# Kernel tuning notes

Hardware: AMD Instinct MI355X
Metric: run time of the kernel (lower is better)

The kernel has to match this reference:

```python
import jax, jax.numpy as jnp
import numpy as np

T = 5
EPS = 1e-05


def setup_inputs() -> dict:
    key = jax.random.key(0)
    X = jax.random.normal(key, (64, 512, 32, 32), dtype=jnp.float32)
    return {"X": X}


def reference(X):
    # IterNorm (training branch): whiten channels via Newton-Schulz inverse sqrt.
    N, C, H, W = X.shape
    x = jnp.transpose(X, (1, 0, 2, 3)).reshape(C, -1)  # [d, m], d=C, m=N*H*W
    d, m = x.shape
    mean = jnp.mean(x, axis=-1, keepdims=True)
    xc = x - mean
    I = jnp.eye(d, dtype=X.dtype)
    # Sigma = eps*I + (1/m) xc xc^T  (addmm(eps, I, 1/m, xc, xc^T))
    Sigma = EPS * I + (xc @ xc.T) / m
    rTr = 1.0 / jnp.trace(Sigma)          # (Sigma * I).sum().reciprocal()
    Sigma_N = Sigma * rTr
    P = I
    for _ in range(T):
        # P_{k+1} = 1.5*P_k - 0.5 * P_k^3 @ Sigma_N
        P = 1.5 * P - 0.5 * (P @ P @ P) @ Sigma_N
    wm = P * jnp.sqrt(rTr)                # whitening matrix ~ Sigma^{-1/2}
    xn = wm @ xc                          # [d, m]
    Xn = jnp.transpose(xn.reshape(C, N, H, W), (1, 0, 2, 3))
    return Xn
```

## Files before the change

kernel.cpp:

```cpp
#include <hip/hip_runtime.h>
#include <math.h>

#define Nn   64
#define Cc   512
#define HWs  1024
#define CHW  (Cc * HWs)
#define Mm   (Nn * HWs)
#define EPSC 1e-5f
#define NBC  128

typedef unsigned int   u32;
typedef unsigned short u16;
typedef __attribute__((ext_vector_type(8))) short  short8;
typedef __attribute__((ext_vector_type(4))) float  floatx4;

__device__ __forceinline__ u16 f2bf(float f) {
    u32 u = __float_as_uint(f);
    u += 0x7fff + ((u >> 16) & 1);
    return (u16)(u >> 16);
}
__device__ __forceinline__ float bf2f(u16 h) {
    return __uint_as_float(((u32)h) << 16);
}

__device__ __forceinline__ void gld_lds16(const u16* g, u16* l) {
    __builtin_amdgcn_global_load_lds(
        (const __attribute__((address_space(1))) u32*)g,
        (__attribute__((address_space(3))) u32*)l, 16, 0, 0);
}

__global__ __launch_bounds__(256) void convert_transpose(const float* __restrict__ X,
                                                         u16* __restrict__ Xbf,
                                                         u16* __restrict__ Xt,
                                                         float* __restrict__ meanP) {
    const int hT = blockIdx.x;
    const int h0 = hT << 6;
    const int c0 = blockIdx.y << 6;
    const int n  = blockIdx.z;
    const int t  = threadIdx.x;
    __shared__ u16   T[64][65];
    __shared__ float red[64][17];

    const float* Xn  = X   + (size_t)n * CHW;
    u16*         Xbn = Xbf + (size_t)n * CHW;
    u16*         Xtn = Xt  + (size_t)n * CHW;

    const int cl = t >> 4;
    const int h4 = (t & 15) << 2;
#pragma unroll
    for (int i = 0; i < 4; ++i) {
        const int c = cl + (i << 4);
        float4 v = *(const float4*)&Xn[(size_t)(c0 + c) * HWs + h0 + h4];
        red[c][t & 15] = v.x + v.y + v.z + v.w;
        u16 b0 = f2bf(v.x), b1 = f2bf(v.y), b2 = f2bf(v.z), b3 = f2bf(v.w);
        *(ushort4*)&Xbn[(size_t)(c0 + c) * HWs + h0 + h4] = make_ushort4(b0, b1, b2, b3);
        T[c][h4]     = b0;
        T[c][h4 + 1] = b1;
        T[c][h4 + 2] = b2;
        T[c][h4 + 3] = b3;
    }
    __syncthreads();
    const int hl = t >> 4;
    const int c4 = (t & 15) << 2;
#pragma unroll
    for (int i = 0; i < 4; ++i) {
        const int h = hl + (i << 4);
        ushort4 pk = make_ushort4(T[c4][h], T[c4 + 1][h], T[c4 + 2][h], T[c4 + 3][h]);
        *(ushort4*)&Xtn[(size_t)(h0 + h) * Cc + c0 + c4] = pk;
    }
    if (t < 64) {
        float s = 0.f;
#pragma unroll
        for (int j = 0; j < 16; ++j) s += red[t][j];
        atomicAdd(&meanP[hT * 512 + c0 + t], s);
    }
}

__global__ __launch_bounds__(256) void gram_mfma(const u16* __restrict__ Xbf,
                                                 float* __restrict__ G) {
    static const int TI[10] = {0,0,0,0,1,1,1,2,2,3};
    static const int TJ[10] = {0,1,2,3,1,2,3,2,3,3};
    const int id = blockIdx.x;
    const int q  = id >> 3;
    const int x  = q % 10;
    const int y  = (id & 7) + ((q / 10) << 3);
    const int i0 = TI[x] << 7;
    const int j0 = TJ[x] << 7;
    const int n  = y;
    const int t  = threadIdx.x;
    const int w  = t >> 6, l = t & 63;

    __shared__ u16 As[2][4096];
    __shared__ u16 Bs[2][4096];

    floatx4 acc[4][4];
#pragma unroll
    for (int mi = 0; mi < 4; ++mi)
#pragma unroll
        for (int ni = 0; ni < 4; ++ni) acc[mi][ni] = (floatx4){0.f, 0.f, 0.f, 0.f};

    const int lr = l >> 2;
    const int lc = (l & 3) << 3;
    const int wm = w >> 1, wn = w & 1;
    const int fm = l & 15, fq = l >> 4;

    const u16* Xn = Xbf + (size_t)n * CHW;

    auto issue = [&](int k, int bb) {
#pragma unroll
        for (int p = 0; p < 2; ++p) {
            const int g   = w * 2 + p;
            const int row = g * 16 + lr;
            gld_lds16(Xn + (size_t)(i0 + row) * HWs + (k << 5) + lc, &As[bb][g * 512]);
            gld_lds16(Xn + (size_t)(j0 + row) * HWs + (k << 5) + lc, &Bs[bb][g * 512]);
        }
    };

    issue(0, 0);
    __syncthreads();
    for (int k = 0; k < 32; ++k) {
        if (k < 31) issue(k + 1, (k + 1) & 1);
        const int bb = k & 1;
        short8 a[4], b[4];
#pragma unroll
        for (int mi = 0; mi < 4; ++mi)
            a[mi] = *(const short8*)&As[bb][(wm * 64 + mi * 16 + fm) * 32 + fq * 8];
#pragma unroll
        for (int ni = 0; ni < 4; ++ni)
            b[ni] = *(const short8*)&Bs[bb][(wn * 64 + ni * 16 + fm) * 32 + fq * 8];
#pragma unroll
        for (int mi = 0; mi < 4; ++mi)
#pragma unroll
            for (int ni = 0; ni < 4; ++ni)
                acc[mi][ni] = __builtin_amdgcn_mfma_f32_16x16x32_bf16(
                    a[mi], b[ni], acc[mi][ni], 0, 0, 0);
        __syncthreads();
    }
#pragma unroll
    for (int mi = 0; mi < 4; ++mi)
#pragma unroll
        for (int ni = 0; ni < 4; ++ni)
#pragma unroll
            for (int r = 0; r < 4; ++r) {
                const int gi = i0 + wm * 64 + mi * 16 + fq * 4 + r;
                const int gj = j0 + wn * 64 + ni * 16 + fm;
                atomicAdd(&G[(size_t)gi * Cc + gj], acc[mi][ni][r]);
            }
}

__device__ __forceinline__ void gridbar(int* bar, int gen) {
    __syncthreads();
    if (threadIdx.x == 0) {
        __threadfence();
        __hip_atomic_fetch_add(bar, 1, __ATOMIC_RELAXED, __HIP_MEMORY_SCOPE_AGENT);
        while (__hip_atomic_load(bar, __ATOMIC_RELAXED, __HIP_MEMORY_SCOPE_AGENT) < gen * NBC)
            __builtin_amdgcn_s_sleep(1);
        __threadfence();
    }
    __syncthreads();
}

template <int MR>
__device__ __forceinline__ void mm_bk64(const u16* Ah, const u16* Al,
                                        const u16* Bh, const u16* Bl,
                                        int i0, int j0,
                                        float alpha, const float* D, float beta,
                                        float* Cf, u16* Ch, u16* Cl, u16* S) {
    const int t = threadIdx.x, w = t >> 6, l = t & 63;
    const int wm = w >> 1, wn = w & 1, fm = l & 15, fq = l >> 4;
    const int lr = l >> 2, lc = (l & 3) << 3;
    constexpr int MI     = MR / 32;
    constexpr int OFF_AL = MR * 64;
    constexpr int OFF_BH = 2 * MR * 64;
    constexpr int OFF_BL = 2 * MR * 64 + 4096;
    constexpr int BUFSZ  = 2 * MR * 64 + 8192;

    const u16* src  = (w == 0) ? Ah : (w == 1) ? Al : (w == 2) ? Bh : Bl;
    const int rbase = (w < 2) ? i0 : j0;
    const int R     = (w < 2) ? MR : 64;
    const int OFF   = (w == 0) ? 0 : (w == 1) ? OFF_AL : (w == 2) ? OFF_BH : OFF_BL;

    floatx4 acc[MI][2];
#pragma unroll
    for (int mi = 0; mi < MI; ++mi)
#pragma unroll
        for (int ni = 0; ni < 2; ++ni) acc[mi][ni] = (floatx4){0.f, 0.f, 0.f, 0.f};

    auto issue = [&](int c, int bb) {
        u16* dst = S + bb * BUFSZ + OFF;
        const u16* sp = src + (size_t)rbase * 512 + (c << 6);
#pragma unroll
        for (int s = 0; s < 2; ++s)
#pragma unroll 4
            for (int g = 0; g < (R >> 4); ++g)
                gld_lds16(sp + (size_t)(g * 16 + lr) * 512 + s * 32 + lc,
                          dst + s * R * 32 + g * 512);
    };
    auto compute = [&](int bb) {
        const u16* base = S + bb * BUFSZ;
#pragma unroll
        for (int s = 0; s < 2; ++s) {
            short8 ah[MI], al[MI], bh[2], bl[2];
#pragma unroll
            for (int mi = 0; mi < MI; ++mi) {
                const int r = wm * (MR / 2) + mi * 16 + fm;
                const int o = s * MR * 32 + r * 32 + fq * 8;
                ah[mi] = *(const short8*)&base[o];
                al[mi] = *(const short8*)&base[OFF_AL + o];
            }
#pragma unroll
            for (int ni = 0; ni < 2; ++ni) {
                const int r = wn * 32 + ni * 16 + fm;
                const int o = s * 2048 + r * 32 + fq * 8;
                bh[ni] = *(const short8*)&base[OFF_BH + o];
                bl[ni] = *(const short8*)&base[OFF_BL + o];
            }
#pragma unroll
            for (int mi = 0; mi < MI; ++mi)
#pragma unroll
                for (int ni = 0; ni < 2; ++ni) {
                    acc[mi][ni] = __builtin_amdgcn_mfma_f32_16x16x32_bf16(ah[mi], bh[ni], acc[mi][ni], 0, 0, 0);
                    acc[mi][ni] = __builtin_amdgcn_mfma_f32_16x16x32_bf16(ah[mi], bl[ni], acc[mi][ni], 0, 0, 0);
                    acc[mi][ni] = __builtin_amdgcn_mfma_f32_16x16x32_bf16(al[mi], bh[ni], acc[mi][ni], 0, 0, 0);
                }
        }
    };

    issue(0, 0);
    __syncthreads();
    for (int c = 0; c < 8; ++c) {
        if (c < 7) issue(c + 1, (c + 1) & 1);
        compute(c & 1);
        __syncthreads();
    }

#pragma unroll
    for (int mi = 0; mi < MI; ++mi)
#pragma unroll
        for (int ni = 0; ni < 2; ++ni)
#pragma unroll
            for (int r4 = 0; r4 < 4; ++r4) {
                const int gi = i0 + wm * (MR / 2) + mi * 16 + fq * 4 + r4;
                const int gj = j0 + wn * 32 + ni * 16 + fm;
                const size_t idx = (size_t)gi * 512 + gj;
                float v = alpha * acc[mi][ni][r4];
                if (D) v += beta * D[idx];
                if (Cf) Cf[idx] = v;
                const u16 h = f2bf(v);
                Ch[idx] = h;
                Cl[idx] = f2bf(v - bf2f(h));
            }
}

__global__ __launch_bounds__(256) void ns_chain(
    const float* G, const float* meanP, float* scal, int* bar, float* wmmv,
    u16* Sh, u16* Sl, u16* PhA, u16* PlA, u16* PhB, u16* PlB,
    u16* T2h, u16* T2l, u16* Wh, u16* Wl, float* PfA, float* PfB) {
    __shared__ u16   S[32768];
    __shared__ float meanL[512];
    __shared__ float redL[4];
    const int t = threadIdx.x, b = blockIdx.x;
    const int w = t >> 6, l = t & 63;

    float tp = 0.f;
#pragma unroll
    for (int cb = 0; cb < 2; ++cb) {
        const int c = t + (cb << 8);
        float s = 0.f;
#pragma unroll
        for (int q = 0; q < 16; ++q) s += meanP[(q << 9) + c];
        const float mc = s * (1.0f / Mm);
        meanL[c] = mc;
        tp += G[(size_t)c * 513] * (1.0f / Mm) - mc * mc;
    }
#pragma unroll
    for (int o = 32; o > 0; o >>= 1) tp += __shfl_xor(tp, o);
    if (l == 0) redL[w] = tp;
    __syncthreads();
    const float tr  = redL[0] + redL[1] + redL[2] + redL[3] + (float)Cc * EPSC;
    const float rtr = 1.0f / tr;
    const float sr  = sqrtf(rtr);
    if (b == 0 && t == 0) { scal[0] = rtr; scal[1] = sr; }

#pragma unroll
    for (int k2 = 0; k2 < 8; ++k2) {
        const int e = (b << 11) + (k2 << 8) + t;
        const int i = e >> 9, j = e & 511;
        const float g = (i <= j) ? G[((size_t)i << 9) + j] : G[((size_t)j << 9) + i];
        float sig = g * (1.0f / Mm) - meanL[i] * meanL[j];
        if (i == j) sig += EPSC;
        const float sN = sig * rtr;
        const u16 sh = f2bf(sN);
        Sh[e] = sh;
        Sl[e] = f2bf(sN - bf2f(sh));
        const float p1 = ((i == j) ? 1.5f : 0.f) - 0.5f * sN;
        PfA[e] = p1;
        const u16 ph = f2bf(p1);
        PhA[e] = ph;
        PlA[e] = f2bf(p1 - bf2f(ph));
    }
    int gen = 0;
    gridbar(bar, ++gen);

    u16 *ph = PhA, *pl = PlA, *qh = PhB, *ql = PlB;
    float *pf = PfA, *qf = PfB;
    const int i0a = ((b & 63) >> 3) << 6, j0a = (b & 7) << 6;
    const int i0b = (b >> 3) << 5,        j0b = (b & 7) << 6;
    for (int it = 0; it < 4; ++it) {
        if (b < 64)
            mm_bk64<64>(ph, pl, ph, pl, i0a, j0a, 1.f, nullptr, 0.f,
                        nullptr, T2h, T2l, S);
        else
            mm_bk64<64>(ph, pl, Sh, Sl, i0a, j0a, 1.f, nullptr, 0.f,
                        nullptr, Wh, Wl, S);
        gridbar(bar, ++gen);
        mm_bk64<32>(T2h, T2l, Wh, Wl, i0b, j0b, -0.5f, pf, 1.5f,
                    qf, qh, ql, S);
        gridbar(bar, ++gen);
        { u16* x = ph; ph = qh; qh = x; }
        { u16* x = pl; pl = ql; ql = x; }
        { float* x = pf; pf = qf; qf = x; }
    }

    {
        const int c = (b << 2) + (t >> 6);
        float s = 0.f;
#pragma unroll
        for (int jj = 0; jj < 8; ++jj) {
            const int j = l + (jj << 6);
            s += pf[((size_t)c << 9) + j] * meanL[j];
        }
#pragma unroll
        for (int o = 32; o > 0; o >>= 1) s += __shfl_xor(s, o);
        if (l == 0) wmmv[c] = s * sr;
    }
}

__global__ __launch_bounds__(256) void whiten_mfma(const u16* __restrict__ Xt,
                                                   const u16* __restrict__ Pbf,
                                                   const float* __restrict__ wmm,
                                                   const float* __restrict__ scal,
                                                   float* __restrict__ out) {
    const int id  = blockIdx.x;
    const int m   = (id >> 3) & 3;
    const int grp = (id & 7) + ((id >> 5) << 3);
    const int c0  = m << 7;
    const int h0  = (grp & 7) << 7;
    const int n   = grp >> 3;
    const int t   = threadIdx.x;
    const int w   = t >> 6, l = t & 63;

    __shared__ char smem[128 * 68 * 4];
    u16* AsB = (u16*)smem;
    u16* BsB = AsB + 8192;
    float* Ep = (float*)smem;

    floatx4 acc[4][4];
#pragma unroll
    for (int mi = 0; mi < 4; ++mi)
#pragma unroll
        for (int ni = 0; ni < 4; ++ni) acc[mi][ni] = (floatx4){0.f, 0.f, 0.f, 0.f};

    const int lr = l >> 2;
    const int lc = (l & 3) << 3;
    const int wm = w >> 1, wn = w & 1;
    const int fm = l & 15, fq = l >> 4;

    const u16* Xn = Xt + (size_t)n * CHW;

    auto issue = [&](int k, int bb) {
#pragma unroll
        for (int p = 0; p < 2; ++p) {
            const int g   = w * 2 + p;
            const int row = g * 16 + lr;
            gld_lds16(Xn  + (size_t)(h0 + row) * Cc + (k << 5) + lc, &AsB[bb * 4096 + g * 512]);
            gld_lds16(Pbf + (size_t)(c0 + row) * Cc + (k << 5) + lc, &BsB[bb * 4096 + g * 512]);
        }
    };

    issue(0, 0);
    __syncthreads();
    for (int k = 0; k < 16; ++k) {
        if (k < 15) issue(k + 1, (k + 1) & 1);
        const int bb = k & 1;
        short8 a[4], b[4];
#pragma unroll
        for (int mi = 0; mi < 4; ++mi)
            a[mi] = *(const short8*)&AsB[bb * 4096 + (wm * 64 + mi * 16 + fm) * 32 + fq * 8];
#pragma unroll
        for (int ni = 0; ni < 4; ++ni)
            b[ni] = *(const short8*)&BsB[bb * 4096 + (wn * 64 + ni * 16 + fm) * 32 + fq * 8];
#pragma unroll
        for (int mi = 0; mi < 4; ++mi)
#pragma unroll
            for (int ni = 0; ni < 4; ++ni)
                acc[mi][ni] = __builtin_amdgcn_mfma_f32_16x16x32_bf16(
                    a[mi], b[ni], acc[mi][ni], 0, 0, 0);
        __syncthreads();
    }

    const float sr = scal[1];
    float wv[4];
#pragma unroll
    for (int ni = 0; ni < 4; ++ni) wv[ni] = wmm[c0 + wn * 64 + ni * 16 + fm];
    float* outn = out + (size_t)n * CHW;

#pragma unroll
    for (int mp = 0; mp < 2; ++mp) {
        __syncthreads();
#pragma unroll
        for (int p = 0; p < 2; ++p) {
            const int mi = mp * 2 + p;
#pragma unroll
            for (int ni = 0; ni < 4; ++ni) {
                const int row  = wn * 64 + ni * 16 + fm;
                const int slot = wm * 32 + p * 16 + fq * 4;
                floatx4 v = acc[mi][ni] * sr - wv[ni];
                *(floatx4*)&Ep[row * 68 + slot] = v;
            }
        }
        __syncthreads();
#pragma unroll
        for (int jj = 0; jj < 8; ++jj) {
            const int idx = jj * 256 + t;
            const int row = idx >> 4;
            const int s4  = (idx & 15) << 2;
            const int wmr = s4 >> 5;
            const int within = s4 & 31;
            float4 v = *(const float4*)&Ep[row * 68 + s4];
            *(float4*)&outn[(size_t)(c0 + row) * HWs + h0 + wmr * 64 + mp * 32 + within] = v;
        }
    }
}

__global__ __launch_bounds__(256) void mean_kernel(const float* __restrict__ X,
                                                   float* __restrict__ mean) {
    const int c = blockIdx.x;
    const int t = threadIdx.x;
    float s = 0.f;
    for (int n = 0; n < Nn; ++n) {
        const float4* p = (const float4*)(X + (size_t)n * CHW + (size_t)c * HWs);
        float4 v = p[t];
        s += v.x + v.y + v.z + v.w;
    }
    __shared__ float red[256];
    red[t] = s;
    __syncthreads();
    for (int o = 128; o > 0; o >>= 1) {
        if (t < o) red[t] += red[t + o];
        __syncthreads();
    }
    if (t == 0) mean[c] = red[0] * (1.0f / Mm);
}

__global__ __launch_bounds__(256) void trace_fb(const float* __restrict__ G,
                                                const float* __restrict__ mean,
                                                float* __restrict__ scal) {
    const int t = threadIdx.x;
    float s = 0.f;
    for (int i = t; i < Cc; i += 256)
        s += G[(size_t)i * Cc + i] * (1.0f / Mm) - mean[i] * mean[i];
    __shared__ float red[256];
    red[t] = s;
    __syncthreads();
    for (int o = 128; o > 0; o >>= 1) {
        if (t < o) red[t] += red[t + o];
        __syncthreads();
    }
    if (t == 0) {
        const float tr  = red[0] + (float)Cc * EPSC;
        const float rtr = 1.0f / tr;
        scal[0] = rtr;
        scal[1] = sqrtf(rtr);
    }
}

__global__ __launch_bounds__(256) void gram_kernel(const float* __restrict__ X,
                                                   float* __restrict__ G) {
    const int ti = blockIdx.x >> 3, tj = blockIdx.x & 7;
    const int i0 = ti << 6, j0 = tj << 6;
    const int n0 = blockIdx.y << 3;
    const int t  = threadIdx.x;
    const int tx = t & 15, ty = t >> 4;
    __shared__ float As[64][33];
    __shared__ float Bs[64][33];
    float acc[4][4] = {};
    const int lc = t & 31;
    const int lr0 = t >> 5;
    for (int n = n0; n < n0 + 8; ++n) {
        const float* Xn = X + (size_t)n * CHW;
        for (int hw0 = 0; hw0 < HWs; hw0 += 32) {
#pragma unroll
            for (int r = 0; r < 8; ++r) {
                const int row = lr0 + (r << 3);
                As[row][lc] = Xn[(size_t)(i0 + row) * HWs + hw0 + lc];
                Bs[row][lc] = Xn[(size_t)(j0 + row) * HWs + hw0 + lc];
            }
            __syncthreads();
#pragma unroll
            for (int k = 0; k < 32; ++k) {
                float a[4], b[4];
#pragma unroll
                for (int r = 0; r < 4; ++r) a[r] = As[(ty << 2) + r][k];
#pragma unroll
                for (int cn = 0; cn < 4; ++cn) b[cn] = Bs[(tx << 2) + cn][k];
#pragma unroll
                for (int r = 0; r < 4; ++r)
#pragma unroll
                    for (int cn = 0; cn < 4; ++cn) acc[r][cn] += a[r] * b[cn];
            }
            __syncthreads();
        }
    }
#pragma unroll
    for (int r = 0; r < 4; ++r)
#pragma unroll
        for (int cn = 0; cn < 4; ++cn)
            atomicAdd(&G[(size_t)(i0 + (ty << 2) + r) * Cc + j0 + (tx << 2) + cn],
                      acc[r][cn]);
}

__global__ __launch_bounds__(256) void sigman_full_kernel(const float* __restrict__ G,
                                                          const float* __restrict__ mean,
                                                          const float* __restrict__ scal,
                                                          float* __restrict__ S,
                                                          float* __restrict__ P) {
    const int e = blockIdx.x * 256 + threadIdx.x;
    const int i = e >> 9, j = e & 511;
    const float rtr = scal[0];
    float sig = G[e] * (1.0f / Mm) - mean[i] * mean[j];
    if (i == j) sig += EPSC;
    S[e] = sig * rtr;
    P[e] = (i == j) ? 1.f : 0.f;
}

__global__ __launch_bounds__(256) void mm512_kernel(const float* __restrict__ A,
                                                    const float* __restrict__ B,
                                                    float* __restrict__ C,
                                                    float alpha,
                                                    const float* __restrict__ D,
                                                    float beta) {
    const int ti = blockIdx.x >> 3, tj = blockIdx.x & 7;
    const int i0 = ti << 6, j0 = tj << 6;
    const int t  = threadIdx.x;
    const int tx = t & 15, ty = t >> 4;
    __shared__ float As[64][33];
    __shared__ float Bs[32][65];
    float acc[4][4] = {};
    const int lcA = t & 31, lrA = t >> 5;
    const int lcB = t & 63, lrB = t >> 6;
    for (int k0 = 0; k0 < 512; k0 += 32) {
#pragma unroll
        for (int r = 0; r < 8; ++r) {
            const int row = lrA + (r << 3);
            As[row][lcA] = A[(size_t)(i0 + row) * 512 + k0 + lcA];
        }
#pragma unroll
        for (int r = 0; r < 8; ++r) {
            const int row = lrB + (r << 2);
            Bs[row][lcB] = B[(size_t)(k0 + row) * 512 + j0 + lcB];
        }
        __syncthreads();
#pragma unroll
        for (int k = 0; k < 32; ++k) {
            float a[4], b[4];
#pragma unroll
            for (int r = 0; r < 4; ++r) a[r] = As[(ty << 2) + r][k];
#pragma unroll
            for (int cn = 0; cn < 4; ++cn) b[cn] = Bs[k][(tx << 2) + cn];
#pragma unroll
            for (int r = 0; r < 4; ++r)
#pragma unroll
                for (int cn = 0; cn < 4; ++cn) acc[r][cn] += a[r] * b[cn];
        }
        __syncthreads();
    }
#pragma unroll
    for (int r = 0; r < 4; ++r) {
        const size_t idx = (size_t)(i0 + (ty << 2) + r) * 512 + j0 + (tx << 2);
        float4 v;
        v.x = alpha * acc[r][0];
        v.y = alpha * acc[r][1];
        v.z = alpha * acc[r][2];
        v.w = alpha * acc[r][3];
        if (D) {
            const float4 d = *(const float4*)(D + idx);
            v.x += beta * d.x; v.y += beta * d.y; v.z += beta * d.z; v.w += beta * d.w;
        }
        *(float4*)(C + idx) = v;
    }
}

__global__ __launch_bounds__(128) void wmm_kernel(const float* __restrict__ P,
                                                  const float* __restrict__ mean,
                                                  const float* __restrict__ scal,
                                                  float* __restrict__ wmm) {
    const int c = blockIdx.x, t = threadIdx.x;
    float s = 0.f;
    for (int j = t; j < Cc; j += 128) s += P[(size_t)c * Cc + j] * mean[j];
    __shared__ float red[128];
    red[t] = s;
    __syncthreads();
    for (int o = 64; o > 0; o >>= 1) {
        if (t < o) red[t] += red[t + o];
        __syncthreads();
    }
    if (t == 0) wmm[c] = red[0] * scal[1];
}

__global__ __launch_bounds__(256) void whiten_kernel(const float* __restrict__ X,
                                                     const float* __restrict__ P,
                                                     const float* __restrict__ wmm,
                                                     const float* __restrict__ scal,
                                                     float* __restrict__ out) {
    const int c0 = blockIdx.x << 6;
    const int h0 = blockIdx.y << 6;
    const int n  = blockIdx.z;
    const int t  = threadIdx.x;
    const int tx = t & 15, ty = t >> 4;
    __shared__ float Ps[64][33];
    __shared__ float Xs[32][65];
    float acc[4][4] = {};
    const int lcA = t & 31, lrA = t >> 5;
    const int lcB = t & 63, lrB = t >> 6;
    const float* Xn = X + (size_t)n * CHW;
    for (int k0 = 0; k0 < 512; k0 += 32) {
#pragma unroll
        for (int r = 0; r < 8; ++r) {
            const int row = lrA + (r << 3);
            Ps[row][lcA] = P[(size_t)(c0 + row) * 512 + k0 + lcA];
        }
#pragma unroll
        for (int r = 0; r < 8; ++r) {
            const int row = lrB + (r << 2);
            Xs[row][lcB] = Xn[(size_t)(k0 + row) * HWs + h0 + lcB];
        }
        __syncthreads();
#pragma unroll
        for (int k = 0; k < 32; ++k) {
            float a[4], b[4];
#pragma unroll
            for (int r = 0; r < 4; ++r) a[r] = Ps[(ty << 2) + r][k];
#pragma unroll
            for (int cn = 0; cn < 4; ++cn) b[cn] = Xs[k][(tx << 2) + cn];
#pragma unroll
            for (int r = 0; r < 4; ++r)
#pragma unroll
                for (int cn = 0; cn < 4; ++cn) acc[r][cn] += a[r] * b[cn];
        }
        __syncthreads();
    }
    const float sr = scal[1];
#pragma unroll
    for (int r = 0; r < 4; ++r) {
        const int c = c0 + (ty << 2) + r;
        const float wv = wmm[c];
        float4 v;
        v.x = sr * acc[r][0] - wv;
        v.y = sr * acc[r][1] - wv;
        v.z = sr * acc[r][2] - wv;
        v.w = sr * acc[r][3] - wv;
        *(float4*)(out + (size_t)n * CHW + (size_t)c * HWs + h0 + (tx << 2)) = v;
    }
}

extern "C" void kernel_launch(void* const* d_in, const int* in_sizes, int n_in,
                              void* d_out, int out_size, void* d_ws, size_t ws_size,
                              hipStream_t stream) {
    const float* X = (const float*)d_in[0];
    float* out     = (float*)d_out;

    const size_t NU16 = 33554432;
    const size_t NM   = 262144;
    const size_t NEED = NU16 * 2 * 2
                      + NM * 10 * 2
                      + (NM + 8192 + 32 + 512 + 512 + 2 * NM) * 4;

    if (ws_size >= NEED) {
        u16* Xbf = (u16*)d_ws;
        u16* Xt  = Xbf + NU16;
        u16* Sh  = Xt  + NU16;
        u16* Sl  = Sh + NM;
        u16* PhA = Sl + NM;
        u16* PlA = PhA + NM;
        u16* PhB = PlA + NM;
        u16* PlB = PhB + NM;
        u16* T2h = PlB + NM;
        u16* T2l = T2h + NM;
        u16* Wh  = T2l + NM;
        u16* Wl  = Wh + NM;
        float* G     = (float*)(Wl + NM);
        float* meanP = G + NM;
        float* scal  = meanP + 8192;
        int*   bar   = (int*)(scal + 16);
        float* mean  = (float*)(bar + 16);
        float* wmm   = mean + 512;
        float* PfA   = wmm + 512;
        float* PfB   = PfA + NM;

        hipMemsetAsync(G, 0, (NM + 8192 + 32) * sizeof(float), stream);
        convert_transpose<<<dim3(16, 8, 64), 256, 0, stream>>>(X, Xbf, Xt, meanP);
        gram_mfma<<<640, 256, 0, stream>>>(Xbf, G);
        ns_chain<<<NBC, 256, 0, stream>>>(G, meanP, scal, bar, wmm,
                                          Sh, Sl, PhA, PlA, PhB, PlB,
                                          T2h, T2l, Wh, Wl, PfA, PfB);
        whiten_mfma<<<2048, 256, 0, stream>>>(Xt, PhA, wmm, scal, out);
    } else {
        float* ws   = (float*)d_ws;
        float* mean = ws;
        float* wmm  = ws + 512;
        float* scal = ws + 1024;
        float* G    = ws + 2048;
        float* S    = G + 262144;
        float* Pa   = S + 262144;
        float* Pb   = Pa + 262144;
        float* P2   = Pb + 262144;
        float* P3   = P2 + 262144;

        mean_kernel<<<512, 256, 0, stream>>>(X, mean);
        hipMemsetAsync(G, 0, sizeof(float) * 262144, stream);
        gram_kernel<<<dim3(64, 8), 256, 0, stream>>>(X, G);
        trace_fb<<<1, 256, 0, stream>>>(G, mean, scal);
        sigman_full_kernel<<<1024, 256, 0, stream>>>(G, mean, scal, S, Pa);

        float* P  = Pa;
        float* Pn = Pb;
        for (int it = 0; it < 5; ++it) {
            mm512_kernel<<<64, 256, 0, stream>>>(P, P, P2, 1.f, nullptr, 0.f);
            mm512_kernel<<<64, 256, 0, stream>>>(P2, P, P3, 1.f, nullptr, 0.f);
            mm512_kernel<<<64, 256, 0, stream>>>(P3, S, Pn, -0.5f, P, 1.5f);
            float* tmp = P; P = Pn; Pn = tmp;
        }

        wmm_kernel<<<512, 128, 0, stream>>>(P, mean, scal, wmm);
        whiten_kernel<<<dim3(8, 16, 64), 256, 0, stream>>>(X, P, wmm, scal, out);
    }
}
```

Measured before the change: 524.0 us.

## Replace grid-barrier fences with cache-bypassing loads/stores and packed transposed stores

```diff
diff --git a/kernel.cpp b/kernel.cpp
--- a/kernel.cpp
+++ b/kernel.cpp
@@ -11,6 +11,7 @@
 
 typedef unsigned int   u32;
 typedef unsigned short u16;
+typedef unsigned long long u64;
 typedef __attribute__((ext_vector_type(8))) short  short8;
 typedef __attribute__((ext_vector_type(4))) float  floatx4;
 
@@ -27,6 +28,21 @@
     __builtin_amdgcn_global_load_lds(
         (const __attribute__((address_space(1))) u32*)g,
         (__attribute__((address_space(3))) u32*)l, 16, 0, 0);
+}
+
+#define AUX_SC 0x11
+
+__device__ __forceinline__ void gld_lds16_sc(const u16* g, u16* l) {
+    __builtin_amdgcn_global_load_lds(
+        (const __attribute__((address_space(1))) u32*)g,
+        (__attribute__((address_space(3))) u32*)l, 16, 0, AUX_SC);
+}
+__device__ __forceinline__ void st8_sc(u16* p, u64 pk) {
+    asm volatile("global_store_dwordx2 %0, %1, off sc0 sc1"
+                 :: "v"(p), "v"(pk) : "memory");
+}
+__device__ __forceinline__ u64 pk4(const u16* h) {
+    return (u64)h[0] | ((u64)h[1] << 16) | ((u64)h[2] << 32) | ((u64)h[3] << 48);
 }
 
 __global__ __launch_bounds__(256) void convert_transpose(const float* __restrict__ X,
@@ -149,13 +165,12 @@
 }
 
 __device__ __forceinline__ void gridbar(int* bar, int gen) {
+    asm volatile("s_waitcnt vmcnt(0)" ::: "memory");
     __syncthreads();
     if (threadIdx.x == 0) {
-        __threadfence();
         __hip_atomic_fetch_add(bar, 1, __ATOMIC_RELAXED, __HIP_MEMORY_SCOPE_AGENT);
         while (__hip_atomic_load(bar, __ATOMIC_RELAXED, __HIP_MEMORY_SCOPE_AGENT) < gen * NBC)
             __builtin_amdgcn_s_sleep(1);
-        __threadfence();
     }
     __syncthreads();
 }
@@ -193,8 +208,8 @@
         for (int s = 0; s < 2; ++s)
 #pragma unroll 4
             for (int g = 0; g < (R >> 4); ++g)
-                gld_lds16(sp + (size_t)(g * 16 + lr) * 512 + s * 32 + lc,
-                          dst + s * R * 32 + g * 512);
+                gld_lds16_sc(sp + (size_t)(g * 16 + lr) * 512 + s * 32 + lc,
+                             dst + s * R * 32 + g * 512);
     };
     auto compute = [&](int bb) {
         const u16* base = S + bb * BUFSZ;
@@ -237,19 +252,21 @@
 #pragma unroll
     for (int mi = 0; mi < MI; ++mi)
 #pragma unroll
-        for (int ni = 0; ni < 2; ++ni)
+        for (int ni = 0; ni < 2; ++ni) {
+            const int gib = i0 + wm * (MR / 2) + mi * 16 + fq * 4;
+            const int gj  = j0 + wn * 32 + ni * 16 + fm;
+            u16 h[4], lo[4];
 #pragma unroll
             for (int r4 = 0; r4 < 4; ++r4) {
-                const int gi = i0 + wm * (MR / 2) + mi * 16 + fq * 4 + r4;
-                const int gj = j0 + wn * 32 + ni * 16 + fm;
-                const size_t idx = (size_t)gi * 512 + gj;
                 float v = alpha * acc[mi][ni][r4];
-                if (D) v += beta * D[idx];
-                if (Cf) Cf[idx] = v;
-                const u16 h = f2bf(v);
-                Ch[idx] = h;
-                Cl[idx] = f2bf(v - bf2f(h));
+                if (D) v += beta * D[(size_t)(gib + r4) * 512 + gj];
+                if (Cf) Cf[(size_t)(gib + r4) * 512 + gj] = v;
+                h[r4]  = f2bf(v);
+                lo[r4] = f2bf(v - bf2f(h[r4]));
             }
+            st8_sc(&Ch[(size_t)gj * 512 + gib], pk4(h));
+            st8_sc(&Cl[(size_t)gj * 512 + gib], pk4(lo));
+        }
 }
 
 __global__ __launch_bounds__(256) void ns_chain(
@@ -282,22 +299,34 @@
     const float sr  = sqrtf(rtr);
     if (b == 0 && t == 0) { scal[0] = rtr; scal[1] = sr; }
 
-#pragma unroll
-    for (int k2 = 0; k2 < 8; ++k2) {
-        const int e = (b << 11) + (k2 << 8) + t;
-        const int i = e >> 9, j = e & 511;
-        const float g = (i <= j) ? G[((size_t)i << 9) + j] : G[((size_t)j << 9) + i];
-        float sig = g * (1.0f / Mm) - meanL[i] * meanL[j];
-        if (i == j) sig += EPSC;
-        const float sN = sig * rtr;
-        const u16 sh = f2bf(sN);
-        Sh[e] = sh;
-        Sl[e] = f2bf(sN - bf2f(sh));
-        const float p1 = ((i == j) ? 1.5f : 0.f) - 0.5f * sN;
-        PfA[e] = p1;
-        const u16 ph = f2bf(p1);
-        PhA[e] = ph;
-        PlA[e] = f2bf(p1 - bf2f(ph));
+    const int R0 = (b >> 3) << 5;
+    const int C0 = (b & 7) << 6;
+#pragma unroll
+    for (int k2 = 0; k2 < 2; ++k2) {
+        const int idx4 = (k2 << 8) + t;
+        const int i  = R0 + (idx4 >> 4);
+        const int jb = C0 + ((idx4 & 15) << 2);
+        float p1[4];
+        u16 sh[4], sl[4], ph[4], pl[4];
+#pragma unroll
+        for (int u = 0; u < 4; ++u) {
+            const int j = jb + u;
+            const float g = (i <= j) ? G[((size_t)i << 9) + j] : G[((size_t)j << 9) + i];
+            float sig = g * (1.0f / Mm) - meanL[i] * meanL[j];
+            if (i == j) sig += EPSC;
+            const float sN = sig * rtr;
+            sh[u] = f2bf(sN);
+            sl[u] = f2bf(sN - bf2f(sh[u]));
+            p1[u] = ((i == j) ? 1.5f : 0.f) - 0.5f * sN;
+            ph[u] = f2bf(p1[u]);
+            pl[u] = f2bf(p1[u] - bf2f(ph[u]));
+        }
+        const size_t e = ((size_t)i << 9) + jb;
+        st8_sc(&Sh[e],  pk4(sh));
+        st8_sc(&Sl[e],  pk4(sl));
+        st8_sc(&PhA[e], pk4(ph));
+        st8_sc(&PlA[e], pk4(pl));
+        *(float4*)&PfA[e] = make_float4(p1[0], p1[1], p1[2], p1[3]);
     }
     int gen = 0;
     gridbar(bar, ++gen);
@@ -305,7 +334,6 @@
     u16 *ph = PhA, *pl = PlA, *qh = PhB, *ql = PlB;
     float *pf = PfA, *qf = PfB;
     const int i0a = ((b & 63) >> 3) << 6, j0a = (b & 7) << 6;
-    const int i0b = (b >> 3) << 5,        j0b = (b & 7) << 6;
     for (int it = 0; it < 4; ++it) {
         if (b < 64)
             mm_bk64<64>(ph, pl, ph, pl, i0a, j0a, 1.f, nullptr, 0.f,
@@ -314,7 +342,7 @@
             mm_bk64<64>(ph, pl, Sh, Sl, i0a, j0a, 1.f, nullptr, 0.f,
                         nullptr, Wh, Wl, S);
         gridbar(bar, ++gen);
-        mm_bk64<32>(T2h, T2l, Wh, Wl, i0b, j0b, -0.5f, pf, 1.5f,
+        mm_bk64<32>(T2h, T2l, Wh, Wl, R0, C0, -0.5f, pf, 1.5f,
                     qf, qh, ql, S);
         gridbar(bar, ++gen);
         { u16* x = ph; ph = qh; qh = x; }
@@ -323,16 +351,16 @@
     }
 
     {
-        const int c = (b << 2) + (t >> 6);
+        const int row = R0 + (t >> 3);
+        const int jb  = C0 + ((t & 7) << 3);
         float s = 0.f;
 #pragma unroll
-        for (int jj = 0; jj < 8; ++jj) {
-            const int j = l + (jj << 6);
-            s += pf[((size_t)c << 9) + j] * meanL[j];
-        }
-#pragma unroll
-        for (int o = 32; o > 0; o >>= 1) s += __shfl_xor(s, o);
-        if (l == 0) wmmv[c] = s * sr;
+        for (int jj = 0; jj < 8; ++jj)
+            s += pf[((size_t)row << 9) + jb + jj] * meanL[jb + jj];
+        s += __shfl_xor(s, 1);
+        s += __shfl_xor(s, 2);
+        s += __shfl_xor(s, 4);
+        if ((t & 7) == 0) atomicAdd(&wmmv[row], s * sr);
     }
 }
 
@@ -698,7 +726,7 @@
         float* PfA   = wmm + 512;
         float* PfB   = PfA + NM;
 
-        hipMemsetAsync(G, 0, (NM + 8192 + 32) * sizeof(float), stream);
+        hipMemsetAsync(G, 0, (NM + 8192 + 32 + 1024) * sizeof(float), stream);
         convert_transpose<<<dim3(16, 8, 64), 256, 0, stream>>>(X, Xbf, Xt, meanP);
         gram_mfma<<<640, 256, 0, stream>>>(Xbf, G);
         ns_chain<<<NBC, 256, 0, stream>>>(G, meanP, scal, bar, wmm,
```

Result: faster. 467.7 us (-10.7%).
